# Kernel optimization log

Hardware: AMD Instinct MI355X
Metric: run time of the kernel (lower is better)

## Reference

```python
import jax, jax.numpy as jnp
import numpy as np
from jax import lax

B, CIN, L = 2048, 1024, 30
E, C = 8, 2            # num_experts, num_classes
FC_IN = 256 * 9        # 2304
FIN_IN = C + 512 * L + 256 * (L // 2 + 1)  # 19458


def _maxpool1d(x):
    # MaxPool1d(kernel=2, stride=2, padding=1); pad with -inf like torch
    return lax.reduce_window(x, -jnp.inf, lax.max,
                             (1, 1, 2), (1, 1, 2),
                             [(0, 0), (0, 0), (1, 1)])


def _conv1d(x, w):
    # x: [B,Cin,L], w: [Cout,Cin,3], padding=1
    return lax.conv_general_dilated(x, w, (1,), [(1, 1)],
                                    dimension_numbers=('NCH', 'OIH', 'NCH'))


def setup_inputs() -> dict:
    key = jax.random.key(0)
    ks = jax.random.split(key, 16)
    s = 0.02
    inp = {
        'x': jax.random.normal(ks[0], (B, CIN, L), jnp.float32),
        'expert_idx': jax.random.randint(ks[1], (B,), 0, E),
        'conv1_w': jax.random.normal(ks[2], (512, 1024, 3), jnp.float32) * s,
        'conv1_b': jnp.zeros((512,), jnp.float32),
        'conv2_w': jax.random.normal(ks[3], (256, 512, 3), jnp.float32) * s,
        'conv2_b': jnp.zeros((256,), jnp.float32),
        'fc_w': jax.random.normal(ks[4], (1024, FC_IN), jnp.float32) * s,
        'fc_b': jnp.zeros((1024,), jnp.float32),
        'e_w1': jax.random.normal(ks[5], (E, 512, 1024), jnp.float32) * s,
        'e_b1': jnp.zeros((E, 512), jnp.float32),
        'e_w2': jax.random.normal(ks[6], (E, C, 512), jnp.float32) * s,
        'e_b2': jnp.zeros((E, C), jnp.float32),
        'agg_w': jax.random.normal(ks[7], (C, E * C), jnp.float32) * s,
        'agg_b': jnp.zeros((C,), jnp.float32),
        'fin_w': jax.random.normal(ks[8], (C, FIN_IN), jnp.float32) * s,
        'fin_b': jnp.zeros((C,), jnp.float32),
    }
    return inp


def reference(x, expert_idx, conv1_w, conv1_b, conv2_w, conv2_b, fc_w, fc_b,
              e_w1, e_b1, e_w2, e_b2, agg_w, agg_b, fin_w, fin_b):
    b = x.shape[0]
    # shared feature extractor
    x1 = jax.nn.relu(_conv1d(x, conv1_w) + conv1_b[None, :, None])     # [B,512,30]
    p1 = _maxpool1d(x1)                                                 # [B,512,16]
    x2 = jax.nn.relu(_conv1d(p1, conv2_w) + conv2_b[None, :, None])    # [B,256,16]
    p2 = _maxpool1d(x2)                                                 # [B,256,9]
    sf = jax.nn.relu(p2.reshape(b, -1) @ fc_w.T + fc_b)                 # [B,1024]

    # expert dispatch: run all experts densely, then select per-sample
    h = jax.nn.relu(jnp.einsum('bd,ehd->beh', sf, e_w1) + e_b1)        # [B,E,512]
    all_out = jnp.einsum('beh,ech->bec', h, e_w2) + e_b2               # [B,E,C]
    sel = all_out[jnp.arange(b), expert_idx]                           # [B,C]
    oh = jax.nn.one_hot(expert_idx, E, dtype=sel.dtype)                # [B,E]
    expert_outputs = (oh[:, :, None] * sel[:, None, :]).reshape(b, E * C)

    agg = expert_outputs @ agg_w.T + agg_b                             # [B,C]
    combined = jnp.concatenate(
        [agg, x1.reshape(b, -1), x2.reshape(b, -1)], axis=1)           # [B,19458]
    return combined @ fin_w.T + fin_b                                  # [B,C]
```

## Files before the change

kernel.cpp:

```cpp
#include <hip/hip_runtime.h>
#include <hip/hip_bf16.h>

typedef short short8 __attribute__((ext_vector_type(8)));
typedef short short4v __attribute__((ext_vector_type(4)));
typedef float f32x4 __attribute__((ext_vector_type(4)));

__device__ __forceinline__ float bf2f(short s) {
  return __builtin_bit_cast(float, (unsigned)((unsigned short)s) << 16);
}
__device__ __forceinline__ short f2bf(float f) {
  return __builtin_bit_cast(short, __float2bfloat16(f));
}
__device__ __forceinline__ void g2lds16(const void* g, void* l) {
  __builtin_amdgcn_global_load_lds((const __attribute__((address_space(1))) void*)g,
                                   (__attribute__((address_space(3))) void*)l, 16, 0, 0);
}


__global__ __launch_bounds__(256) void prep_x(const float* __restrict__ x, short* __restrict__ xt) {
  __shared__ float tile[64 * 30];
  const int b = blockIdx.x, ci0 = blockIdx.y * 64, t = threadIdx.x;
  const float* src = x + ((long)b * 1024 + ci0) * 30;
  for (int i = t; i < 1920; i += 256) tile[i] = src[i];
  __syncthreads();
  short* dst = xt + (long)b * 32 * 1024 + ci0;
  for (int i = t; i < 2048; i += 256) {
    int lp = i >> 6, ci = i & 63;
    float v = (lp == 0 || lp == 31) ? 0.f : tile[ci * 30 + lp - 1];
    dst[(long)lp * 1024 + ci] = f2bf(v);
  }
}

__global__ __launch_bounds__(256) void prep_weights(
    const float* __restrict__ conv1_w, const float* __restrict__ conv2_w,
    const float* __restrict__ fc_w, const float* __restrict__ e_w1,
    const float* __restrict__ fin_w,
    short* __restrict__ w1t, short* __restrict__ w2t, short* __restrict__ fcwt,
    short* __restrict__ ew1t, float* __restrict__ finw1, float* __restrict__ finw2) {
  const int T0 = 1572864;
  const int T1 = T0 + 393216;
  const int T2 = T1 + 2359296;
  const int T3 = T2 + 4194304;
  const int T4 = T3 + 30720;
  const int T5 = T4 + 8192;
  for (long idx = (long)blockIdx.x * 256 + threadIdx.x; idx < T5;
       idx += (long)gridDim.x * 256) {
    if (idx < T0) {
      int i = (int)idx; int co = i / 3072, j = i % 3072, k = j >> 10, ci = j & 1023;
      w1t[i] = f2bf(conv1_w[(co * 1024 + ci) * 3 + k]);
    } else if (idx < T1) {
      int i = (int)(idx - T0); int co = i / 1536, j = i % 1536, k = j >> 9, ci = j & 511;
      w2t[i] = f2bf(conv2_w[(co * 512 + ci) * 3 + k]);
    } else if (idx < T2) {
      int i = (int)(idx - T1); int n = i / 2304, j = i % 2304, jj = j >> 8, co = j & 255;
      fcwt[i] = f2bf(fc_w[n * 2304 + co * 9 + jj]);
    } else if (idx < T3) {
      int i = (int)(idx - T2);
      ew1t[i] = f2bf(e_w1[i]);
    } else if (idx < T4) {
      int i = (int)(idx - T3); int c = i / 15360, r = i % 15360, l = r >> 9, co = r & 511;
      finw1[i] = fin_w[c * 19458 + 2 + co * 30 + l];
    } else {
      int i = (int)(idx - T4); int c = i / 4096, r = i % 4096, l = r >> 8, co = r & 255;
      finw2[i] = fin_w[c * 19458 + 2 + 15360 + co * 16 + l];
    }
  }
}

__global__ __launch_bounds__(512, 2) void gemm256_bt_relu(
    const short* __restrict__ A, const short* __restrict__ Bm, short* __restrict__ C,
    const float* __restrict__ bias, int N, int K, int L, int S1, int S2, int nNB) {
  __shared__ __align__(16) short lA0[256 * 64], lA1[256 * 64];
  __shared__ __align__(16) short lB0[256 * 64], lB1[256 * 64];
  const int t = threadIdx.x, wave = t >> 6, lane = t & 63;
  const int wr = wave >> 2, wc = wave & 3;
  const int nwg = gridDim.x, qn = nwg >> 3, bid = blockIdx.x;
  const int swz = (bid & 7) * qn + (bid >> 3);
  const int m0 = (swz / nNB) * 256, n0 = (swz % nNB) * 256;
  const int srow = t >> 3;
  const int scol = ((t & 7) ^ (srow & 7)) * 8;

  long aoff[4], boff[4];
#pragma unroll
  for (int q = 0; q < 4; ++q) {
    int m = m0 + q * 64 + srow;
    aoff[q] = (long)(m / L) * S1 + (long)(m % L) * S2 + scol;
    boff[q] = (long)(n0 + q * 64 + srow) * K + scol;
  }
  const int ldst = wave * 512 + lane * 8;

  f32x4 acc[8][4];
#pragma unroll
  for (int i = 0; i < 8; ++i)
#pragma unroll
    for (int j = 0; j < 4; ++j) acc[i][j] = f32x4{0.f, 0.f, 0.f, 0.f};

  const int l7 = lane & 7, g4 = lane >> 4, r16 = lane & 15;
  const int nK = K >> 6;

#define STAGE256(k0, dA, dB) do {                                     \
    const long kk0_ = (long)(k0);                                     \
    _Pragma("unroll")                                                 \
    for (int q = 0; q < 4; ++q) {                                     \
      g2lds16(A + aoff[q] + kk0_, &dA[q * 4096 + ldst]);              \
      g2lds16(Bm + boff[q] + kk0_, &dB[q * 4096 + ldst]);             \
    } } while (0)

#define PHASES256(sA, sB) do {                                                        \
    short8 af[4][2], bfr[4][2];                                                       \
                                 \
    _Pragma("unroll") for (int kk = 0; kk < 2; ++kk) {                                \
      const int jb = ((kk * 4 + g4) ^ l7) * 8;                                        \
      _Pragma("unroll") for (int i = 0; i < 4; ++i)                                   \
        af[i][kk] = *(const short8*)&sA[(wr * 128 + i * 16 + r16) * 64 + jb];         \
      _Pragma("unroll") for (int j = 0; j < 2; ++j)                                   \
        bfr[j][kk] = *(const short8*)&sB[(wc * 64 + j * 16 + r16) * 64 + jb];         \
    }                                                                                 \
    __builtin_amdgcn_s_setprio(1);                                                    \
    _Pragma("unroll") for (int i = 0; i < 4; ++i)                                     \
    _Pragma("unroll") for (int j = 0; j < 2; ++j)                                     \
    _Pragma("unroll") for (int kk = 0; kk < 2; ++kk)                                  \
      acc[i][j] = __builtin_amdgcn_mfma_f32_16x16x32_bf16(af[i][kk], bfr[j][kk], acc[i][j], 0, 0, 0); \
    __builtin_amdgcn_s_setprio(0);                                                    \
                                         \
    _Pragma("unroll") for (int kk = 0; kk < 2; ++kk) {                                \
      const int jb = ((kk * 4 + g4) ^ l7) * 8;                                        \
      _Pragma("unroll") for (int j = 0; j < 2; ++j)                                   \
        bfr[2 + j][kk] = *(const short8*)&sB[(wc * 64 + (2 + j) * 16 + r16) * 64 + jb]; \
    }                                                                                 \
    __builtin_amdgcn_s_setprio(1);                                                    \
    _Pragma("unroll") for (int i = 0; i < 4; ++i)                                     \
    _Pragma("unroll") for (int j = 0; j < 2; ++j)                                     \
    _Pragma("unroll") for (int kk = 0; kk < 2; ++kk)                                  \
      acc[i][2 + j] = __builtin_amdgcn_mfma_f32_16x16x32_bf16(af[i][kk], bfr[2 + j][kk], acc[i][2 + j], 0, 0, 0); \
    __builtin_amdgcn_s_setprio(0);                                                    \
                                         \
    _Pragma("unroll") for (int kk = 0; kk < 2; ++kk) {                                \
      const int jb = ((kk * 4 + g4) ^ l7) * 8;                                        \
      _Pragma("unroll") for (int i = 0; i < 4; ++i)                                   \
        af[i][kk] = *(const short8*)&sA[(wr * 128 + (4 + i) * 16 + r16) * 64 + jb];   \
    }                                                                                 \
    __builtin_amdgcn_s_setprio(1);                                                    \
    _Pragma("unroll") for (int i = 0; i < 4; ++i)                                     \
    _Pragma("unroll") for (int j = 0; j < 2; ++j)                                     \
    _Pragma("unroll") for (int kk = 0; kk < 2; ++kk)                                  \
      acc[4 + i][2 + j] = __builtin_amdgcn_mfma_f32_16x16x32_bf16(af[i][kk], bfr[2 + j][kk], acc[4 + i][2 + j], 0, 0, 0); \
    __builtin_amdgcn_s_setprio(0);                                                    \
                                \
    __builtin_amdgcn_s_setprio(1);                                                    \
    _Pragma("unroll") for (int i = 0; i < 4; ++i)                                     \
    _Pragma("unroll") for (int j = 0; j < 2; ++j)                                     \
    _Pragma("unroll") for (int kk = 0; kk < 2; ++kk)                                  \
      acc[4 + i][j] = __builtin_amdgcn_mfma_f32_16x16x32_bf16(af[i][kk], bfr[j][kk], acc[4 + i][j], 0, 0, 0); \
    __builtin_amdgcn_s_setprio(0);                                                    \
  } while (0)

  STAGE256(0, lA0, lB0);
  for (int ktp = 0; ktp < (nK >> 1); ++ktp) {
    const int t1 = 2 * ktp + 1;
    __syncthreads();
    STAGE256((long)t1 << 6, lA1, lB1);
    PHASES256(lA0, lB0);
    __syncthreads();
    if (t1 + 1 < nK) STAGE256((long)(t1 + 1) << 6, lA0, lB0);
    PHASES256(lA1, lB1);
  }

#pragma unroll
  for (int j = 0; j < 4; ++j) {
    int col = n0 + wc * 64 + j * 16 + r16;
    float bv = bias[col];
#pragma unroll
    for (int i = 0; i < 8; ++i) {
      int rbase = m0 + wr * 128 + i * 16 + (g4 << 2);
#pragma unroll
      for (int r = 0; r < 4; ++r) {
        float o = fmaxf(acc[i][j][r] + bv, 0.f);
        C[(long)(rbase + r) * N + col] = f2bf(o);
      }
    }
  }
#undef STAGE256
#undef PHASES256
}

__global__ __launch_bounds__(256) void gemm_bt_relu(
    const short* __restrict__ A, const short* __restrict__ Bm, short* __restrict__ C,
    const float* __restrict__ bias, int N, int K, int L, int S1, int S2, int nNB) {
  __shared__ __align__(16) short lA[128 * 64];
  __shared__ __align__(16) short lB[128 * 64];
  const int t = threadIdx.x, wave = t >> 6, lane = t & 63;
  const int wr = wave >> 1, wc = wave & 1;
  const int nwg = gridDim.x, q = nwg >> 3, bid = blockIdx.x;
  const int swz = (bid & 7) * q + (bid >> 3);
  const int m0 = (swz / nNB) * 128, n0 = (swz % nNB) * 128;
  const int arow = t >> 3;
  const int sw8 = arow & 7;
  const int acolg = (((t & 7) ^ sw8) * 8);

  long aoff[4], boff[4];
#pragma unroll
  for (int qq = 0; qq < 4; ++qq) {
    int m = m0 + qq * 32 + arow;
    aoff[qq] = (long)(m / L) * S1 + (long)(m % L) * S2 + acolg;
    boff[qq] = (long)(n0 + qq * 32 + arow) * K + acolg;
  }

  f32x4 acc[4][4];
#pragma unroll
  for (int i = 0; i < 4; ++i)
#pragma unroll
    for (int j = 0; j < 4; ++j) acc[i][j] = f32x4{0.f, 0.f, 0.f, 0.f};

  const int l7 = lane & 7, g4 = lane >> 4, r16 = lane & 15;
  const int nK = K >> 6;
  for (int kt = 0; kt < nK; ++kt) {
    const int k0 = kt << 6;
#pragma unroll
    for (int qq = 0; qq < 4; ++qq) {
      g2lds16(A + aoff[qq] + k0, &lA[qq * 2048 + wave * 512 + lane * 8]);
      g2lds16(Bm + boff[qq] + k0, &lB[qq * 2048 + wave * 512 + lane * 8]);
    }
    __syncthreads();
#pragma unroll
    for (int kk = 0; kk < 2; ++kk) {
      const int jblk = ((kk * 4 + g4) ^ l7) * 8;
      short8 af[4], bfv[4];
#pragma unroll
      for (int i = 0; i < 4; ++i)
        af[i] = *(const short8*)&lA[(wr * 64 + i * 16 + r16) * 64 + jblk];
#pragma unroll
      for (int j = 0; j < 4; ++j)
        bfv[j] = *(const short8*)&lB[(wc * 64 + j * 16 + r16) * 64 + jblk];
#pragma unroll
      for (int i = 0; i < 4; ++i)
#pragma unroll
        for (int j = 0; j < 4; ++j)
          acc[i][j] = __builtin_amdgcn_mfma_f32_16x16x32_bf16(af[i], bfv[j], acc[i][j], 0, 0, 0);
    }
    __syncthreads();
  }

#pragma unroll
  for (int j = 0; j < 4; ++j) {
    int col = n0 + wc * 64 + j * 16 + (lane & 15);
    float bv = bias[col];
#pragma unroll
    for (int i = 0; i < 4; ++i) {
      int rbase = m0 + wr * 64 + i * 16 + ((lane >> 4) << 2);
#pragma unroll
      for (int r = 0; r < 4; ++r) {
        float o = fmaxf(acc[i][j][r] + bv, 0.f);
        C[(long)(rbase + r) * N + col] = f2bf(o);
      }
    }
  }
}

__global__ __launch_bounds__(256) void pool1(const short* __restrict__ x1t, short* __restrict__ p1t) {
  const long total = (long)2048 * 18 * 128;
  for (long idx = (long)blockIdx.x * 256 + threadIdx.x; idx < total;
       idx += (long)gridDim.x * 256) {
    int c4 = (int)(idx & 127); long tmp = idx >> 7; int jp = (int)(tmp % 18); long b = tmp / 18;
    short4v v = {0, 0, 0, 0};
    if (jp >= 1 && jp <= 16) {
      int j = jp - 1;
      int l0 = 2 * j - 1, l1 = 2 * j;
      short4v a = (l0 >= 0) ? *(const short4v*)&x1t[(b * 30 + l0) * 512 + c4 * 4] : short4v{0, 0, 0, 0};
      short4v bb = (l1 < 30) ? *(const short4v*)&x1t[(b * 30 + l1) * 512 + c4 * 4] : short4v{0, 0, 0, 0};
#pragma unroll
      for (int u = 0; u < 4; ++u) v[u] = f2bf(fmaxf(bf2f(a[u]), bf2f(bb[u])));
    }
    *(short4v*)&p1t[idx * 4] = v;
  }
}

__global__ __launch_bounds__(256) void pool2(const short* __restrict__ x2t, short* __restrict__ p2t) {
  const long total = (long)2048 * 9 * 64;
  for (long idx = (long)blockIdx.x * 256 + threadIdx.x; idx < total;
       idx += (long)gridDim.x * 256) {
    int c4 = (int)(idx & 63); long tmp = idx >> 6; int j = (int)(tmp % 9); long b = tmp / 9;
    int l0 = 2 * j - 1, l1 = 2 * j;
    short4v a = (l0 >= 0) ? *(const short4v*)&x2t[(b * 16 + l0) * 256 + c4 * 4] : short4v{0, 0, 0, 0};
    short4v bb = (l1 < 16) ? *(const short4v*)&x2t[(b * 16 + l1) * 256 + c4 * 4] : short4v{0, 0, 0, 0};
    short4v v;
#pragma unroll
    for (int u = 0; u < 4; ++u) v[u] = f2bf(fmaxf(bf2f(a[u]), bf2f(bb[u])));
    *(short4v*)&p2t[idx * 4] = v;
  }
}

__global__ __launch_bounds__(256) void final_k(
    const short* __restrict__ h, const short* __restrict__ x1t, const short* __restrict__ x2t,
    const int* __restrict__ eidx, const float* __restrict__ e_w2, const float* __restrict__ e_b2,
    const float* __restrict__ agg_w, const float* __restrict__ agg_b,
    const float* __restrict__ fin_w, const float* __restrict__ fin_b,
    const float* __restrict__ finw1, const float* __restrict__ finw2,
    float* __restrict__ out) {
  const int b = blockIdx.x, t = threadIdx.x, lane = t & 63, wave = t >> 6;
  const int e = eidx[b];
  float s0 = 0.f, s1 = 0.f, f0 = 0.f, f1 = 0.f;
  {
    const short* hp = h + (long)b * 4096 + e * 512;
    const float* w20 = e_w2 + (e * 2 + 0) * 512;
    const float* w21 = e_w2 + (e * 2 + 1) * 512;
    for (int i = t; i < 512; i += 256) {
      float hv = bf2f(hp[i]);
      s0 += hv * w20[i];
      s1 += hv * w21[i];
    }
  }
  {
    const short* xp = x1t + (long)b * 15360;
#pragma unroll
    for (int it = 0; it < 15; ++it) {
      int i = (it * 256 + t) * 4;
      short4v xv = *(const short4v*)&xp[i];
      float4 w0 = *(const float4*)&finw1[i];
      float4 w1 = *(const float4*)&finw1[15360 + i];
      float a0 = bf2f(xv[0]), a1 = bf2f(xv[1]), a2 = bf2f(xv[2]), a3 = bf2f(xv[3]);
      f0 += a0 * w0.x + a1 * w0.y + a2 * w0.z + a3 * w0.w;
      f1 += a0 * w1.x + a1 * w1.y + a2 * w1.z + a3 * w1.w;
    }
    const short* x2p = x2t + (long)b * 4096;
#pragma unroll
    for (int it = 0; it < 4; ++it) {
      int i = (it * 256 + t) * 4;
      short4v xv = *(const short4v*)&x2p[i];
      float4 w0 = *(const float4*)&finw2[i];
      float4 w1 = *(const float4*)&finw2[4096 + i];
      float a0 = bf2f(xv[0]), a1 = bf2f(xv[1]), a2 = bf2f(xv[2]), a3 = bf2f(xv[3]);
      f0 += a0 * w0.x + a1 * w0.y + a2 * w0.z + a3 * w0.w;
      f1 += a0 * w1.x + a1 * w1.y + a2 * w1.z + a3 * w1.w;
    }
  }
#pragma unroll
  for (int off = 32; off > 0; off >>= 1) {
    s0 += __shfl_down(s0, off);
    s1 += __shfl_down(s1, off);
    f0 += __shfl_down(f0, off);
    f1 += __shfl_down(f1, off);
  }
  __shared__ float red[4][4];
  if (lane == 0) { red[wave][0] = s0; red[wave][1] = s1; red[wave][2] = f0; red[wave][3] = f1; }
  __syncthreads();
  if (t == 0) {
    float S0 = 0, S1 = 0, F0 = 0, F1 = 0;
    for (int w = 0; w < 4; ++w) { S0 += red[w][0]; S1 += red[w][1]; F0 += red[w][2]; F1 += red[w][3]; }
    float sel0 = S0 + e_b2[e * 2 + 0];
    float sel1 = S1 + e_b2[e * 2 + 1];
    float agg0 = sel0 * agg_w[e * 2] + sel1 * agg_w[e * 2 + 1] + agg_b[0];
    float agg1 = sel0 * agg_w[16 + e * 2] + sel1 * agg_w[16 + e * 2 + 1] + agg_b[1];
    out[b * 2 + 0] = F0 + agg0 * fin_w[0] + agg1 * fin_w[1] + fin_b[0];
    out[b * 2 + 1] = F1 + agg0 * fin_w[19458 + 0] + agg1 * fin_w[19458 + 1] + fin_b[1];
  }
}

extern "C" void kernel_launch(void* const* d_in, const int* in_sizes, int n_in,
                              void* d_out, int out_size, void* d_ws, size_t ws_size,
                              hipStream_t stream) {
  const float* x       = (const float*)d_in[0];
  const int*   eidx    = (const int*)d_in[1];
  const float* conv1_w = (const float*)d_in[2];
  const float* conv1_b = (const float*)d_in[3];
  const float* conv2_w = (const float*)d_in[4];
  const float* conv2_b = (const float*)d_in[5];
  const float* fc_w    = (const float*)d_in[6];
  const float* fc_b    = (const float*)d_in[7];
  const float* e_w1    = (const float*)d_in[8];
  const float* e_b1    = (const float*)d_in[9];
  const float* e_w2    = (const float*)d_in[10];
  const float* e_b2    = (const float*)d_in[11];
  const float* agg_w   = (const float*)d_in[12];
  const float* agg_b   = (const float*)d_in[13];
  const float* fin_w   = (const float*)d_in[14];
  const float* fin_b   = (const float*)d_in[15];
  float* out = (float*)d_out;

  char* ws = (char*)d_ws;
  short* xt    = (short*)(ws + 0L);
  short* x1t   = (short*)(ws + 134217728L);
  short* p1t   = (short*)(ws + 197132288L);
  short* x2t   = (short*)(ws + 234881024L);
  short* p2t   = (short*)(ws + 251658240L);
  short* sf    = (short*)(ws + 261095424L);
  short* h     = (short*)(ws + 265289728L);
  short* w1t   = (short*)(ws + 282066944L);
  short* w2t   = (short*)(ws + 285212672L);
  short* fcwt  = (short*)(ws + 285999104L);
  short* ew1t  = (short*)(ws + 290717696L);
  float* finw1 = (float*)(ws + 299106304L);
  float* finw2 = (float*)(ws + 299229184L);

  prep_weights<<<4096, 256, 0, stream>>>(conv1_w, conv2_w, fc_w, e_w1, fin_w,
                                         w1t, w2t, fcwt, ew1t, finw1, finw2);
  prep_x<<<dim3(2048, 16), 256, 0, stream>>>(x, xt);
  gemm256_bt_relu<<<480, 512, 0, stream>>>(xt, w1t, x1t, conv1_b, 512, 3072, 30, 32768, 1024, 2);
  pool1<<<2048, 256, 0, stream>>>(x1t, p1t);
  gemm_bt_relu<<<512, 256, 0, stream>>>(p1t, w2t, x2t, conv2_b, 256, 1536, 16, 9216, 512, 2);
  pool2<<<1024, 256, 0, stream>>>(x2t, p2t);
  gemm_bt_relu<<<128, 256, 0, stream>>>(p2t, fcwt, sf, fc_b, 1024, 2304, 1, 2304, 0, 8);
  gemm_bt_relu<<<512, 256, 0, stream>>>(sf, ew1t, h, e_b1, 4096, 1024, 1, 1024, 0, 32);
  final_k<<<2048, 256, 0, stream>>>(h, x1t, x2t, eidx, e_w2, e_b2, agg_w, agg_b,
                                    fin_w, fin_b, finw1, finw2, out);
}
```

Before: 445.1 us.

## Halve K-tile depth in 256x256 GEMM and vectorize prep_x stores

The 256x256 bf16 GEMM now stages K in chunks of 32 instead of 64. Its double-buffered LDS use drops from 128KB to 64KB, with a new XOR swizzle for the narrower rows, which could let two workgroups fit per CU as the launch bounds request. The cost is twice as many barrier-separated iterations, with less MFMA work between syncs to hide load latency. Separately, prep_x writes four bf16 values per store instead of one scalar short.

```diff
diff --git a/kernel.cpp b/kernel.cpp
--- a/kernel.cpp
+++ b/kernel.cpp
@@ -24,10 +24,14 @@
   for (int i = t; i < 1920; i += 256) tile[i] = src[i];
   __syncthreads();
   short* dst = xt + (long)b * 32 * 1024 + ci0;
-  for (int i = t; i < 2048; i += 256) {
-    int lp = i >> 6, ci = i & 63;
-    float v = (lp == 0 || lp == 31) ? 0.f : tile[ci * 30 + lp - 1];
-    dst[(long)lp * 1024 + ci] = f2bf(v);
+  for (int i = t; i < 512; i += 256) {
+    int lp = i >> 4, cq = i & 15;
+    short4v v = {0, 0, 0, 0};
+    if (lp >= 1 && lp <= 30) {
+#pragma unroll
+      for (int u = 0; u < 4; ++u) v[u] = f2bf(tile[(cq * 4 + u) * 30 + lp - 1]);
+    }
+    *(short4v*)&dst[(long)lp * 1024 + cq * 4] = v;
   }
 }
 
@@ -70,24 +74,24 @@
 __global__ __launch_bounds__(512, 2) void gemm256_bt_relu(
     const short* __restrict__ A, const short* __restrict__ Bm, short* __restrict__ C,
     const float* __restrict__ bias, int N, int K, int L, int S1, int S2, int nNB) {
-  __shared__ __align__(16) short lA0[256 * 64], lA1[256 * 64];
-  __shared__ __align__(16) short lB0[256 * 64], lB1[256 * 64];
+  __shared__ __align__(16) short lA0[256 * 32], lA1[256 * 32];
+  __shared__ __align__(16) short lB0[256 * 32], lB1[256 * 32];
   const int t = threadIdx.x, wave = t >> 6, lane = t & 63;
   const int wr = wave >> 2, wc = wave & 3;
   const int nwg = gridDim.x, qn = nwg >> 3, bid = blockIdx.x;
   const int swz = (bid & 7) * qn + (bid >> 3);
   const int m0 = (swz / nNB) * 256, n0 = (swz % nNB) * 256;
-  const int srow = t >> 3;
-  const int scol = ((t & 7) ^ (srow & 7)) * 8;
-
-  long aoff[4], boff[4];
-#pragma unroll
-  for (int q = 0; q < 4; ++q) {
-    int m = m0 + q * 64 + srow;
+  const int srow = t >> 2;
+  const int scol = ((t & 3) ^ ((t >> 3) & 3)) * 8;
+
+  long aoff[2], boff[2];
+#pragma unroll
+  for (int q = 0; q < 2; ++q) {
+    int m = m0 + q * 128 + srow;
     aoff[q] = (long)(m / L) * S1 + (long)(m % L) * S2 + scol;
-    boff[q] = (long)(n0 + q * 64 + srow) * K + scol;
-  }
-  const int ldst = wave * 512 + lane * 8;
+    boff[q] = (long)(n0 + q * 128 + srow) * K + scol;
+  }
+  const int ldst = t * 8;
 
   f32x4 acc[8][4];
 #pragma unroll
@@ -95,75 +99,63 @@
 #pragma unroll
     for (int j = 0; j < 4; ++j) acc[i][j] = f32x4{0.f, 0.f, 0.f, 0.f};
 
-  const int l7 = lane & 7, g4 = lane >> 4, r16 = lane & 15;
-  const int nK = K >> 6;
-
-#define STAGE256(k0, dA, dB) do {                                     \
+  const int g4 = lane >> 4, r16 = lane & 15;
+  const int jb = (g4 ^ ((r16 >> 1) & 3)) * 8;
+  const int nK = K >> 5;
+
+#define STAGE32(k0, dA, dB) do {                                      \
     const long kk0_ = (long)(k0);                                     \
     _Pragma("unroll")                                                 \
-    for (int q = 0; q < 4; ++q) {                                     \
+    for (int q = 0; q < 2; ++q) {                                     \
       g2lds16(A + aoff[q] + kk0_, &dA[q * 4096 + ldst]);              \
       g2lds16(Bm + boff[q] + kk0_, &dB[q * 4096 + ldst]);             \
     } } while (0)
 
-#define PHASES256(sA, sB) do {                                                        \
-    short8 af[4][2], bfr[4][2];                                                       \
-                                 \
-    _Pragma("unroll") for (int kk = 0; kk < 2; ++kk) {                                \
-      const int jb = ((kk * 4 + g4) ^ l7) * 8;                                        \
-      _Pragma("unroll") for (int i = 0; i < 4; ++i)                                   \
-        af[i][kk] = *(const short8*)&sA[(wr * 128 + i * 16 + r16) * 64 + jb];         \
-      _Pragma("unroll") for (int j = 0; j < 2; ++j)                                   \
-        bfr[j][kk] = *(const short8*)&sB[(wc * 64 + j * 16 + r16) * 64 + jb];         \
-    }                                                                                 \
+#define PHASES32(sA, sB) do {                                                         \
+    short8 af[4], bfr[4];                                                             \
+                               \
+    _Pragma("unroll") for (int i = 0; i < 4; ++i)                                     \
+      af[i] = *(const short8*)&sA[(wr * 128 + i * 16 + r16) * 32 + jb];               \
+    _Pragma("unroll") for (int j = 0; j < 2; ++j)                                     \
+      bfr[j] = *(const short8*)&sB[(wc * 64 + j * 16 + r16) * 32 + jb];               \
     __builtin_amdgcn_s_setprio(1);                                                    \
     _Pragma("unroll") for (int i = 0; i < 4; ++i)                                     \
     _Pragma("unroll") for (int j = 0; j < 2; ++j)                                     \
-    _Pragma("unroll") for (int kk = 0; kk < 2; ++kk)                                  \
-      acc[i][j] = __builtin_amdgcn_mfma_f32_16x16x32_bf16(af[i][kk], bfr[j][kk], acc[i][j], 0, 0, 0); \
+      acc[i][j] = __builtin_amdgcn_mfma_f32_16x16x32_bf16(af[i], bfr[j], acc[i][j], 0, 0, 0); \
     __builtin_amdgcn_s_setprio(0);                                                    \
                                          \
-    _Pragma("unroll") for (int kk = 0; kk < 2; ++kk) {                                \
-      const int jb = ((kk * 4 + g4) ^ l7) * 8;                                        \
-      _Pragma("unroll") for (int j = 0; j < 2; ++j)                                   \
-        bfr[2 + j][kk] = *(const short8*)&sB[(wc * 64 + (2 + j) * 16 + r16) * 64 + jb]; \
-    }                                                                                 \
+    _Pragma("unroll") for (int j = 2; j < 4; ++j)                                     \
+      bfr[j] = *(const short8*)&sB[(wc * 64 + j * 16 + r16) * 32 + jb];               \
     __builtin_amdgcn_s_setprio(1);                                                    \
     _Pragma("unroll") for (int i = 0; i < 4; ++i)                                     \
     _Pragma("unroll") for (int j = 0; j < 2; ++j)                                     \
-    _Pragma("unroll") for (int kk = 0; kk < 2; ++kk)                                  \
-      acc[i][2 + j] = __builtin_amdgcn_mfma_f32_16x16x32_bf16(af[i][kk], bfr[2 + j][kk], acc[i][2 + j], 0, 0, 0); \
+      acc[i][2 + j] = __builtin_amdgcn_mfma_f32_16x16x32_bf16(af[i], bfr[2 + j], acc[i][2 + j], 0, 0, 0); \
     __builtin_amdgcn_s_setprio(0);                                                    \
                                          \
-    _Pragma("unroll") for (int kk = 0; kk < 2; ++kk) {                                \
-      const int jb = ((kk * 4 + g4) ^ l7) * 8;                                        \
-      _Pragma("unroll") for (int i = 0; i < 4; ++i)                                   \
-        af[i][kk] = *(const short8*)&sA[(wr * 128 + (4 + i) * 16 + r16) * 64 + jb];   \
-    }                                                                                 \
+    _Pragma("unroll") for (int i = 0; i < 4; ++i)                                     \
+      af[i] = *(const short8*)&sA[(wr * 128 + (4 + i) * 16 + r16) * 32 + jb];         \
     __builtin_amdgcn_s_setprio(1);                                                    \
     _Pragma("unroll") for (int i = 0; i < 4; ++i)                                     \
     _Pragma("unroll") for (int j = 0; j < 2; ++j)                                     \
-    _Pragma("unroll") for (int kk = 0; kk < 2; ++kk)                                  \
-      acc[4 + i][2 + j] = __builtin_amdgcn_mfma_f32_16x16x32_bf16(af[i][kk], bfr[2 + j][kk], acc[4 + i][2 + j], 0, 0, 0); \
+      acc[4 + i][2 + j] = __builtin_amdgcn_mfma_f32_16x16x32_bf16(af[i], bfr[2 + j], acc[4 + i][2 + j], 0, 0, 0); \
     __builtin_amdgcn_s_setprio(0);                                                    \
-                                \
+                              \
     __builtin_amdgcn_s_setprio(1);                                                    \
     _Pragma("unroll") for (int i = 0; i < 4; ++i)                                     \
     _Pragma("unroll") for (int j = 0; j < 2; ++j)                                     \
-    _Pragma("unroll") for (int kk = 0; kk < 2; ++kk)                                  \
-      acc[4 + i][j] = __builtin_amdgcn_mfma_f32_16x16x32_bf16(af[i][kk], bfr[j][kk], acc[4 + i][j], 0, 0, 0); \
+      acc[4 + i][j] = __builtin_amdgcn_mfma_f32_16x16x32_bf16(af[i], bfr[j], acc[4 + i][j], 0, 0, 0); \
     __builtin_amdgcn_s_setprio(0);                                                    \
   } while (0)
 
-  STAGE256(0, lA0, lB0);
+  STAGE32(0, lA0, lB0);
   for (int ktp = 0; ktp < (nK >> 1); ++ktp) {
     const int t1 = 2 * ktp + 1;
     __syncthreads();
-    STAGE256((long)t1 << 6, lA1, lB1);
-    PHASES256(lA0, lB0);
+    STAGE32((long)t1 << 5, lA1, lB1);
+    PHASES32(lA0, lB0);
     __syncthreads();
-    if (t1 + 1 < nK) STAGE256((long)(t1 + 1) << 6, lA0, lB0);
-    PHASES256(lA1, lB1);
+    if (t1 + 1 < nK) STAGE32((long)(t1 + 1) << 5, lA0, lB0);
+    PHASES32(lA1, lB1);
   }
 
 #pragma unroll
@@ -180,8 +172,8 @@
       }
     }
   }
-#undef STAGE256
-#undef PHASES256
+#undef STAGE32
+#undef PHASES32
 }
 
 __global__ __launch_bounds__(256) void gemm_bt_relu(
```

Result: slower. 492.9 us (+10.7%).

## Load GEMM B fragments directly from global memory and vectorize x transpose

Applied to the files above, without the earlier changes.

The 256x256 GEMM kernel no longer stages the B (weight) tile through LDS. Each wave now loads its B fragments straight from global memory into registers right before the MFMA phases, which halves LDS use and removes the LDS reads for B. The trade-off is exposed global-load latency inside the compute loop, since the B loads are issued synchronously with no prefetch, plus redundant B traffic across the two wave rows. Separately, the x transpose/pad kernel writes four bf16 values per store instead of one.

```diff
diff --git a/kernel.cpp b/kernel.cpp
--- a/kernel.cpp
+++ b/kernel.cpp
@@ -24,10 +24,14 @@
   for (int i = t; i < 1920; i += 256) tile[i] = src[i];
   __syncthreads();
   short* dst = xt + (long)b * 32 * 1024 + ci0;
-  for (int i = t; i < 2048; i += 256) {
-    int lp = i >> 6, ci = i & 63;
-    float v = (lp == 0 || lp == 31) ? 0.f : tile[ci * 30 + lp - 1];
-    dst[(long)lp * 1024 + ci] = f2bf(v);
+  for (int i = t; i < 512; i += 256) {
+    int lp = i >> 4, cq = i & 15;
+    short4v v = {0, 0, 0, 0};
+    if (lp >= 1 && lp <= 30) {
+#pragma unroll
+      for (int u = 0; u < 4; ++u) v[u] = f2bf(tile[(cq * 4 + u) * 30 + lp - 1]);
+    }
+    *(short4v*)&dst[(long)lp * 1024 + cq * 4] = v;
   }
 }
 
@@ -71,50 +75,57 @@
     const short* __restrict__ A, const short* __restrict__ Bm, short* __restrict__ C,
     const float* __restrict__ bias, int N, int K, int L, int S1, int S2, int nNB) {
   __shared__ __align__(16) short lA0[256 * 64], lA1[256 * 64];
-  __shared__ __align__(16) short lB0[256 * 64], lB1[256 * 64];
   const int t = threadIdx.x, wave = t >> 6, lane = t & 63;
   const int wr = wave >> 2, wc = wave & 3;
   const int nwg = gridDim.x, qn = nwg >> 3, bid = blockIdx.x;
   const int swz = (bid & 7) * qn + (bid >> 3);
   const int m0 = (swz / nNB) * 256, n0 = (swz % nNB) * 256;
   const int srow = t >> 3;
-  const int scol = ((t & 7) ^ (srow & 7)) * 8;
-
-  long aoff[4], boff[4];
+  const int scol = (((t & 7) ^ (srow & 7)) * 8);
+
+  long aoff[4];
 #pragma unroll
   for (int q = 0; q < 4; ++q) {
     int m = m0 + q * 64 + srow;
     aoff[q] = (long)(m / L) * S1 + (long)(m % L) * S2 + scol;
-    boff[q] = (long)(n0 + q * 64 + srow) * K + scol;
   }
   const int ldst = wave * 512 + lane * 8;
 
+  const int l7 = lane & 7, g4 = lane >> 4, r16 = lane & 15;
+  long brow[4];
+#pragma unroll
+  for (int j = 0; j < 4; ++j)
+    brow[j] = (long)(n0 + wc * 64 + j * 16 + r16) * K + g4 * 8;
+
   f32x4 acc[8][4];
 #pragma unroll
   for (int i = 0; i < 8; ++i)
 #pragma unroll
     for (int j = 0; j < 4; ++j) acc[i][j] = f32x4{0.f, 0.f, 0.f, 0.f};
 
-  const int l7 = lane & 7, g4 = lane >> 4, r16 = lane & 15;
   const int nK = K >> 6;
 
-#define STAGE256(k0, dA, dB) do {                                     \
+#define STAGEA(k0, dA) do {                                           \
     const long kk0_ = (long)(k0);                                     \
     _Pragma("unroll")                                                 \
-    for (int q = 0; q < 4; ++q) {                                     \
+    for (int q = 0; q < 4; ++q)                                       \
       g2lds16(A + aoff[q] + kk0_, &dA[q * 4096 + ldst]);              \
-      g2lds16(Bm + boff[q] + kk0_, &dB[q * 4096 + ldst]);             \
-    } } while (0)
-
-#define PHASES256(sA, sB) do {                                                        \
-    short8 af[4][2], bfr[4][2];                                                       \
-                                 \
+    } while (0)
+
+#define LOADB(k0, bfr) do {                                           \
+    const long kb_ = (long)(k0);                                      \
+    _Pragma("unroll") for (int j = 0; j < 4; ++j)                     \
+    _Pragma("unroll") for (int kk = 0; kk < 2; ++kk)                  \
+      bfr[j][kk] = *(const short8*)&Bm[brow[j] + kb_ + kk * 32];      \
+    } while (0)
+
+#define PHASESA(sA, bfr) do {                                                         \
+    short8 af[4][2];                                                                  \
+                                         \
     _Pragma("unroll") for (int kk = 0; kk < 2; ++kk) {                                \
       const int jb = ((kk * 4 + g4) ^ l7) * 8;                                        \
       _Pragma("unroll") for (int i = 0; i < 4; ++i)                                   \
         af[i][kk] = *(const short8*)&sA[(wr * 128 + i * 16 + r16) * 64 + jb];         \
-      _Pragma("unroll") for (int j = 0; j < 2; ++j)                                   \
-        bfr[j][kk] = *(const short8*)&sB[(wc * 64 + j * 16 + r16) * 64 + jb];         \
     }                                                                                 \
     __builtin_amdgcn_s_setprio(1);                                                    \
     _Pragma("unroll") for (int i = 0; i < 4; ++i)                                     \
@@ -122,12 +133,7 @@
     _Pragma("unroll") for (int kk = 0; kk < 2; ++kk)                                  \
       acc[i][j] = __builtin_amdgcn_mfma_f32_16x16x32_bf16(af[i][kk], bfr[j][kk], acc[i][j], 0, 0, 0); \
     __builtin_amdgcn_s_setprio(0);                                                    \
-                                         \
-    _Pragma("unroll") for (int kk = 0; kk < 2; ++kk) {                                \
-      const int jb = ((kk * 4 + g4) ^ l7) * 8;                                        \
-      _Pragma("unroll") for (int j = 0; j < 2; ++j)                                   \
-        bfr[2 + j][kk] = *(const short8*)&sB[(wc * 64 + (2 + j) * 16 + r16) * 64 + jb]; \
-    }                                                                                 \
+                                                       \
     __builtin_amdgcn_s_setprio(1);                                                    \
     _Pragma("unroll") for (int i = 0; i < 4; ++i)                                     \
     _Pragma("unroll") for (int j = 0; j < 2; ++j)                                     \
@@ -146,7 +152,7 @@
     _Pragma("unroll") for (int kk = 0; kk < 2; ++kk)                                  \
       acc[4 + i][2 + j] = __builtin_amdgcn_mfma_f32_16x16x32_bf16(af[i][kk], bfr[2 + j][kk], acc[4 + i][2 + j], 0, 0, 0); \
     __builtin_amdgcn_s_setprio(0);                                                    \
-                                \
+                                                       \
     __builtin_amdgcn_s_setprio(1);                                                    \
     _Pragma("unroll") for (int i = 0; i < 4; ++i)                                     \
     _Pragma("unroll") for (int j = 0; j < 2; ++j)                                     \
@@ -155,15 +161,18 @@
     __builtin_amdgcn_s_setprio(0);                                                    \
   } while (0)
 
-  STAGE256(0, lA0, lB0);
+  STAGEA(0, lA0);
   for (int ktp = 0; ktp < (nK >> 1); ++ktp) {
     const int t1 = 2 * ktp + 1;
+    short8 bfr[4][2];
     __syncthreads();
-    STAGE256((long)t1 << 6, lA1, lB1);
-    PHASES256(lA0, lB0);
+    STAGEA((long)t1 << 6, lA1);
+    LOADB((long)(2 * ktp) << 6, bfr);
+    PHASESA(lA0, bfr);
     __syncthreads();
-    if (t1 + 1 < nK) STAGE256((long)(t1 + 1) << 6, lA0, lB0);
-    PHASES256(lA1, lB1);
+    if (t1 + 1 < nK) STAGEA((long)(t1 + 1) << 6, lA0);
+    LOADB((long)t1 << 6, bfr);
+    PHASESA(lA1, bfr);
   }
 
 #pragma unroll
@@ -180,8 +189,9 @@
       }
     }
   }
-#undef STAGE256
-#undef PHASES256
+#undef STAGEA
+#undef LOADB
+#undef PHASESA
 }
 
 __global__ __launch_bounds__(256) void gemm_bt_relu(
```

New measurement: 583.9 us. +31.2%, slower.

## Rework 256-tile GEMM pipeline with explicit vmcnt waits and phase barriers

Applied to the files above, without the earlier changes.

The 256x256 bf16 GEMM main loop is restructured. The prefetch of the next K tile into the alternate LDS buffer is now issued at the start of each tile. A partial `s_waitcnt vmcnt(8)` waits only for the previous stage's loads instead of a full `__syncthreads`, and explicit `s_barrier`s with sched_barriers are placed between the MFMA phases to keep waves in lockstep. The loop is peeled so the final tile drains with vmcnt(0). Separately, the input-transpose kernel now writes four bf16 values per store instead of one. The hand-placed waits and barriers rely on exact load counts and risk ordering errors or extra stalls.

```diff
diff --git a/kernel.cpp b/kernel.cpp
--- a/kernel.cpp
+++ b/kernel.cpp
@@ -24,10 +24,14 @@
   for (int i = t; i < 1920; i += 256) tile[i] = src[i];
   __syncthreads();
   short* dst = xt + (long)b * 32 * 1024 + ci0;
-  for (int i = t; i < 2048; i += 256) {
-    int lp = i >> 6, ci = i & 63;
-    float v = (lp == 0 || lp == 31) ? 0.f : tile[ci * 30 + lp - 1];
-    dst[(long)lp * 1024 + ci] = f2bf(v);
+  for (int i = t; i < 512; i += 256) {
+    int lp = i >> 4, cq = i & 15;
+    short4v v = {0, 0, 0, 0};
+    if (lp >= 1 && lp <= 30) {
+#pragma unroll
+      for (int u = 0; u < 4; ++u) v[u] = f2bf(tile[(cq * 4 + u) * 30 + lp - 1]);
+    }
+    *(short4v*)&dst[(long)lp * 1024 + cq * 4] = v;
   }
 }
 
@@ -78,7 +82,7 @@
   const int swz = (bid & 7) * qn + (bid >> 3);
   const int m0 = (swz / nNB) * 256, n0 = (swz % nNB) * 256;
   const int srow = t >> 3;
-  const int scol = ((t & 7) ^ (srow & 7)) * 8;
+  const int scol = (((t & 7) ^ (srow & 7)) * 8);
 
   long aoff[4], boff[4];
 #pragma unroll
@@ -98,7 +102,10 @@
   const int l7 = lane & 7, g4 = lane >> 4, r16 = lane & 15;
   const int nK = K >> 6;
 
-#define STAGE256(k0, dA, dB) do {                                     \
+#define SBAR do { __builtin_amdgcn_sched_barrier(0); __builtin_amdgcn_s_barrier(); \
+                  __builtin_amdgcn_sched_barrier(0); } while (0)
+
+#define STAGE8(k0, dA, dB) do {                                       \
     const long kk0_ = (long)(k0);                                     \
     _Pragma("unroll")                                                 \
     for (int q = 0; q < 4; ++q) {                                     \
@@ -106,21 +113,29 @@
       g2lds16(Bm + boff[q] + kk0_, &dB[q * 4096 + ldst]);             \
     } } while (0)
 
-#define PHASES256(sA, sB) do {                                                        \
-    short8 af[4][2], bfr[4][2];                                                       \
-                                 \
+#define MFMAQ(afr, bfr, IOFF, JOFF)                                                   \
+    _Pragma("unroll") for (int i = 0; i < 4; ++i)                                     \
+    _Pragma("unroll") for (int j = 0; j < 2; ++j)                                     \
+    _Pragma("unroll") for (int kk = 0; kk < 2; ++kk)                                  \
+      acc[(IOFF) + i][(JOFF) + j] = __builtin_amdgcn_mfma_f32_16x16x32_bf16(          \
+          afr[i][kk], bfr[(JOFF) + j][kk], acc[(IOFF) + i][(JOFF) + j], 0, 0, 0)
+
+#define TILE256(sA, sB, STG, VMW)                                                     \
+  do {                                                                                \
+    short8 afr[4][2], bfr[4][2];                                                      \
+    STG;                                                                              \
+    VMW;                                                                              \
+    SBAR;                                                          \
+                                          \
     _Pragma("unroll") for (int kk = 0; kk < 2; ++kk) {                                \
       const int jb = ((kk * 4 + g4) ^ l7) * 8;                                        \
       _Pragma("unroll") for (int i = 0; i < 4; ++i)                                   \
-        af[i][kk] = *(const short8*)&sA[(wr * 128 + i * 16 + r16) * 64 + jb];         \
+        afr[i][kk] = *(const short8*)&sA[(wr * 128 + i * 16 + r16) * 64 + jb];        \
       _Pragma("unroll") for (int j = 0; j < 2; ++j)                                   \
         bfr[j][kk] = *(const short8*)&sB[(wc * 64 + j * 16 + r16) * 64 + jb];         \
     }                                                                                 \
     __builtin_amdgcn_s_setprio(1);                                                    \
-    _Pragma("unroll") for (int i = 0; i < 4; ++i)                                     \
-    _Pragma("unroll") for (int j = 0; j < 2; ++j)                                     \
-    _Pragma("unroll") for (int kk = 0; kk < 2; ++kk)                                  \
-      acc[i][j] = __builtin_amdgcn_mfma_f32_16x16x32_bf16(af[i][kk], bfr[j][kk], acc[i][j], 0, 0, 0); \
+    MFMAQ(afr, bfr, 0, 0);                                                            \
     __builtin_amdgcn_s_setprio(0);                                                    \
                                          \
     _Pragma("unroll") for (int kk = 0; kk < 2; ++kk) {                                \
@@ -128,43 +143,38 @@
       _Pragma("unroll") for (int j = 0; j < 2; ++j)                                   \
         bfr[2 + j][kk] = *(const short8*)&sB[(wc * 64 + (2 + j) * 16 + r16) * 64 + jb]; \
     }                                                                                 \
+    SBAR;                                                                             \
     __builtin_amdgcn_s_setprio(1);                                                    \
-    _Pragma("unroll") for (int i = 0; i < 4; ++i)                                     \
-    _Pragma("unroll") for (int j = 0; j < 2; ++j)                                     \
-    _Pragma("unroll") for (int kk = 0; kk < 2; ++kk)                                  \
-      acc[i][2 + j] = __builtin_amdgcn_mfma_f32_16x16x32_bf16(af[i][kk], bfr[2 + j][kk], acc[i][2 + j], 0, 0, 0); \
+    MFMAQ(afr, bfr, 0, 2);                                                            \
     __builtin_amdgcn_s_setprio(0);                                                    \
-                                         \
+                                       \
     _Pragma("unroll") for (int kk = 0; kk < 2; ++kk) {                                \
       const int jb = ((kk * 4 + g4) ^ l7) * 8;                                        \
       _Pragma("unroll") for (int i = 0; i < 4; ++i)                                   \
-        af[i][kk] = *(const short8*)&sA[(wr * 128 + (4 + i) * 16 + r16) * 64 + jb];   \
+        afr[i][kk] = *(const short8*)&sA[(wr * 128 + (4 + i) * 16 + r16) * 64 + jb];  \
     }                                                                                 \
+    SBAR;                                                                             \
     __builtin_amdgcn_s_setprio(1);                                                    \
-    _Pragma("unroll") for (int i = 0; i < 4; ++i)                                     \
-    _Pragma("unroll") for (int j = 0; j < 2; ++j)                                     \
-    _Pragma("unroll") for (int kk = 0; kk < 2; ++kk)                                  \
-      acc[4 + i][2 + j] = __builtin_amdgcn_mfma_f32_16x16x32_bf16(af[i][kk], bfr[2 + j][kk], acc[4 + i][2 + j], 0, 0, 0); \
+    MFMAQ(afr, bfr, 4, 2);                                                            \
     __builtin_amdgcn_s_setprio(0);                                                    \
-                                \
+                                                       \
+    SBAR;                                                                             \
     __builtin_amdgcn_s_setprio(1);                                                    \
-    _Pragma("unroll") for (int i = 0; i < 4; ++i)                                     \
-    _Pragma("unroll") for (int j = 0; j < 2; ++j)                                     \
-    _Pragma("unroll") for (int kk = 0; kk < 2; ++kk)                                  \
-      acc[4 + i][j] = __builtin_amdgcn_mfma_f32_16x16x32_bf16(af[i][kk], bfr[j][kk], acc[4 + i][j], 0, 0, 0); \
+    MFMAQ(afr, bfr, 4, 0);                                                            \
     __builtin_amdgcn_s_setprio(0);                                                    \
   } while (0)
 
-  STAGE256(0, lA0, lB0);
-  for (int ktp = 0; ktp < (nK >> 1); ++ktp) {
-    const int t1 = 2 * ktp + 1;
-    __syncthreads();
-    STAGE256((long)t1 << 6, lA1, lB1);
-    PHASES256(lA0, lB0);
-    __syncthreads();
-    if (t1 + 1 < nK) STAGE256((long)(t1 + 1) << 6, lA0, lB0);
-    PHASES256(lA1, lB1);
-  }
+#define VM8 asm volatile("s_waitcnt vmcnt(8)" ::: "memory")
+#define VM0 asm volatile("s_waitcnt vmcnt(0)" ::: "memory")
+
+  STAGE8(0, lA0, lB0);
+  for (int ktp = 0; ktp < (nK >> 1) - 1; ++ktp) {
+    const long ke = (long)(2 * ktp);
+    TILE256(lA0, lB0, STAGE8((ke + 1) << 6, lA1, lB1), VM8);
+    TILE256(lA1, lB1, STAGE8((ke + 2) << 6, lA0, lB0), VM8);
+  }
+  TILE256(lA0, lB0, STAGE8((long)(nK - 1) << 6, lA1, lB1), VM8);
+  TILE256(lA1, lB1, (void)0, VM0);
 
 #pragma unroll
   for (int j = 0; j < 4; ++j) {
@@ -180,8 +190,12 @@
       }
     }
   }
-#undef STAGE256
-#undef PHASES256
+#undef SBAR
+#undef STAGE8
+#undef MFMAQ
+#undef TILE256
+#undef VM8
+#undef VM0
 }
 
 __global__ __launch_bounds__(256) void gemm_bt_relu(
```

After: 484.3 us. 8.8% more time.
